# Optimization experiments

Measured on AMD Instinct MI355X. Metric: run time of the kernel, lower is better.

The kernel has to match this reference:

```python
import jax, jax.numpy as jnp
import numpy as np

BEV_X = 128
BEV_Y = 128
NUM_VOXELS = BEV_X * BEV_Y


def setup_inputs() -> dict:
    key = jax.random.key(0)
    k1, k2, k3 = jax.random.split(key, 3)
    B, N, D, H, W, C = 2, 6, 112, 16, 44, 80
    depth_logits = jax.random.normal(k1, (B, N, D, H, W), dtype=jnp.float32)
    context = jax.random.normal(k2, (B, N, C, H, W), dtype=jnp.float32)
    geom_idx = jax.random.randint(k3, (B, N, D, H, W), 0, NUM_VOXELS, dtype=jnp.int32)
    return {"depth_logits": depth_logits, "context": context, "geom_idx": geom_idx}


def reference(depth_logits, context, geom_idx):
    # depth_logits: [B,N,D,H,W], context: [B,N,C,H,W], geom_idx: [B,N,D,H,W] in [0, NUM_VOXELS)
    B, N, D, H, W = depth_logits.shape
    C = context.shape[2]
    # softmax over depth bins -> per-pixel depth distribution
    depth = jax.nn.softmax(depth_logits, axis=2)
    # lift: outer product depth x context -> [B,N,D,H,W,C]
    feat = jnp.einsum('bndhw,bnchw->bndhwc', depth, context)
    P = N * D * H * W
    feat = feat.reshape(B * P, C)
    # splat: scatter-add each frustum point into its BEV voxel (batch-offset indices)
    idx = (geom_idx.reshape(B, P) + jnp.arange(B, dtype=jnp.int32)[:, None] * NUM_VOXELS).reshape(-1)
    bev = jax.ops.segment_sum(feat, idx, num_segments=B * NUM_VOXELS)
    # [B, C, BEV_Y, BEV_X]
    return bev.reshape(B, BEV_Y, BEV_X, C).transpose(0, 3, 1, 2)
```

## Files before the change

### kernel.cpp

```cpp
#include <hip/hip_runtime.h>
#include <hip/hip_bf16.h>


constexpr int B = 2, N = 6, D = 112, H = 16, W = 44, C = 80;
constexpr int HW = H * W;
constexpr int NPIX = B * N * HW;
constexpr int NV = 128 * 128;
constexpr int DHW = D * HW;
constexpr int NBKT = 512;
constexpr int CAP = 2816;
constexpr int RPB = 16 * D;
constexpr int C2 = C / 2;

__device__ inline unsigned bf16rne(float f) {
  const unsigned u = __float_as_uint(f);
  return (u + 0x7FFFu + ((u >> 16) & 1u)) >> 16;
}

__global__ __launch_bounds__(256) void scatter_kernel(
    const float* __restrict__ logits, const float* __restrict__ ctx,
    const int* __restrict__ gidx, unsigned* __restrict__ ctxB,
    int* __restrict__ cursor, unsigned* __restrict__ sorted) {
  const int t = threadIdx.x;
  const int blk = blockIdx.x;
  const int bn = blk / 44;
  const int hw0 = (blk - bn * 44) * 16;
  const int b = bn / N;
  const int pix0 = bn * HW + hw0;

  __shared__ float tile[16][81];
  __shared__ float redm[16][17], reds[16][17];
  __shared__ int hist[256], sbase[256], soff[256];
  __shared__ int wsum[4];
  __shared__ unsigned srec[RPB];
  __shared__ unsigned char sbkt[RPB];

  hist[t] = 0;

  const float* csrc = ctx + (size_t)bn * C * HW + hw0;
#pragma unroll
  for (int it = 0; it < (16 * C) / 256; ++it) {
    const int idx = it * 256 + t;
    const int c = idx >> 4;
    const int i = idx & 15;
    tile[i][c] = csrc[(size_t)c * HW + i];
  }
  __syncthreads();
  {
    unsigned* dst = ctxB + (size_t)pix0 * C2;
    for (int j = t; j < 16 * C2; j += 256) {
      const int p = j / C2;
      const int cp = j - p * C2;
      dst[j] = bf16rne(tile[p][2 * cp]) |
               (bf16rne(tile[p][2 * cp + 1]) << 16);
    }
  }

  const int l = t & 15;
  const int q = t >> 4;
  const size_t base = (size_t)bn * DHW + hw0 + l;

  float x[7];
  float m = -3.0e38f;
#pragma unroll
  for (int j = 0; j < 7; ++j) {
    x[j] = logits[base + (size_t)(q * 7 + j) * HW];
    m = fmaxf(m, x[j]);
  }
  redm[l][q] = m;
  __syncthreads();
#pragma unroll
  for (int qq = 0; qq < 16; ++qq) m = fmaxf(m, redm[l][qq]);
  float s = 0.0f;
#pragma unroll
  for (int j = 0; j < 7; ++j) {
    x[j] = __expf(x[j] - m);
    s += x[j];
  }
  reds[l][q] = s;
  __syncthreads();
  s = 0.0f;
#pragma unroll
  for (int qq = 0; qq < 16; ++qq) s += reds[l][qq];
  const float inv = 1.0f / s;

  unsigned key[7];
  int lb7[7], rank[7];
#pragma unroll
  for (int j = 0; j < 7; ++j) {
    const int fb = b * NV + gidx[base + (size_t)(q * 7 + j) * HW];
    const unsigned p12 = __float2uint_rn(x[j] * inv * 4095.0f);
    key[j] = ((unsigned)(fb & 63) << 26) | ((unsigned)(pix0 + l) << 12) | p12;
    lb7[j] = (fb >> 6) & 255;
    rank[j] = atomicAdd(&hist[lb7[j]], 1);
  }
  __syncthreads();

  const int hv = hist[t];
  int xx = hv;
#pragma unroll
  for (int o = 1; o < 64; o <<= 1) {
    const int y = __shfl_up(xx, o, 64);
    if ((t & 63) >= o) xx += y;
  }
  if ((t & 63) == 63) wsum[t >> 6] = xx;
  sbase[t] = hv ? atomicAdd(&cursor[(b << 8) | t], hv) : 0;
  __syncthreads();
  int woff = 0;
#pragma unroll
  for (int ww = 0; ww < 4; ++ww)
    if (ww < (t >> 6)) woff += wsum[ww];
  soff[t] = woff + xx - hv;
  __syncthreads();

#pragma unroll
  for (int j = 0; j < 7; ++j) {
    const int slot = soff[lb7[j]] + rank[j];
    srec[slot] = key[j];
    sbkt[slot] = (unsigned char)lb7[j];
  }
  __syncthreads();

  for (int s_ = t; s_ < RPB; s_ += 256) {
    const int lb = sbkt[s_];
    const int posin = sbase[lb] + (s_ - soff[lb]);
    if (posin < CAP)
      sorted[(size_t)((b << 8) | lb) * CAP + posin] = srec[s_];
  }
}

__global__ __launch_bounds__(1024) void gather_kernel(
    const unsigned* __restrict__ ctxB, const unsigned* __restrict__ sorted,
    const int* __restrict__ cursor, float* __restrict__ out) {
  const int t = threadIdx.x;
  const int g = blockIdx.x;
  const int b = g >> 8;
  const int vox0 = (g & 255) * 64;

  __shared__ unsigned srec[CAP];
  __shared__ float tile[64][80];
  __shared__ int shist[64], soff[64];

  if (t < 64) shist[t] = 0;
  __syncthreads();

  int cnt = cursor[g];
  if (cnt > CAP) cnt = CAP;
  const unsigned* rec = sorted + (size_t)g * CAP;

  unsigned rr[3];
  int rk[3];
#pragma unroll
  for (int k = 0; k < 3; ++k) {
    const int idx = t + k * 1024;
    rk[k] = -1;
    if (idx < cnt) {
      rr[k] = rec[idx];
      rk[k] = atomicAdd(&shist[rr[k] >> 26], 1);
    }
  }
  __syncthreads();

  if (t < 64) {
    const int v = shist[t];
    int xx = v;
#pragma unroll
    for (int o = 1; o < 64; o <<= 1) {
      const int y = __shfl_up(xx, o, 64);
      if (t >= o) xx += y;
    }
    soff[t] = xx - v;
  }
  __syncthreads();

#pragma unroll
  for (int k = 0; k < 3; ++k) {
    if (rk[k] >= 0) srec[soff[rr[k] >> 26] + rk[k]] = rr[k];
  }
  __syncthreads();

  constexpr float QS = 1.0f / 4095.0f;
  const int w = t >> 6;
  const int l = t & 63;
  for (int j = 0; j < 4; ++j) {
    const int v = w * 4 + j;
    const int s0 = soff[v];
    const int n = shist[v];
    float a0 = 0.0f, a1 = 0.0f;
    int k = 0;
    for (; k + 4 <= n; k += 4) {
      const unsigned ra = srec[s0 + k + 0];
      const unsigned rb = srec[s0 + k + 1];
      const unsigned rc = srec[s0 + k + 2];
      const unsigned rd = srec[s0 + k + 3];
      if (l < C2) {
        const unsigned ua = ctxB[(size_t)((ra >> 12) & 0x3FFFu) * C2 + l];
        const unsigned ub = ctxB[(size_t)((rb >> 12) & 0x3FFFu) * C2 + l];
        const unsigned uc = ctxB[(size_t)((rc >> 12) & 0x3FFFu) * C2 + l];
        const unsigned ud = ctxB[(size_t)((rd >> 12) & 0x3FFFu) * C2 + l];
        const float pa = (float)(ra & 0xFFFu) * QS;
        const float pb = (float)(rb & 0xFFFu) * QS;
        const float pc = (float)(rc & 0xFFFu) * QS;
        const float pd = (float)(rd & 0xFFFu) * QS;
        a0 += pa * __uint_as_float(ua << 16);
        a1 += pa * __uint_as_float(ua & 0xFFFF0000u);
        a0 += pb * __uint_as_float(ub << 16);
        a1 += pb * __uint_as_float(ub & 0xFFFF0000u);
        a0 += pc * __uint_as_float(uc << 16);
        a1 += pc * __uint_as_float(uc & 0xFFFF0000u);
        a0 += pd * __uint_as_float(ud << 16);
        a1 += pd * __uint_as_float(ud & 0xFFFF0000u);
      }
    }
    for (; k < n; ++k) {
      const unsigned ra = srec[s0 + k];
      if (l < C2) {
        const unsigned ua = ctxB[(size_t)((ra >> 12) & 0x3FFFu) * C2 + l];
        const float pa = (float)(ra & 0xFFFu) * QS;
        a0 += pa * __uint_as_float(ua << 16);
        a1 += pa * __uint_as_float(ua & 0xFFFF0000u);
      }
    }
    if (l < C2) {
      tile[v][2 * l] = a0;
      tile[v][2 * l + 1] = a1;
    }
  }
  __syncthreads();

  const size_t ob = (size_t)b * C * NV + vox0;
#pragma unroll
  for (int i = 0; i < 5; ++i) {
    const int idx = i * 1024 + t;
    const int c = idx >> 6;
    const int v = idx & 63;
    out[ob + (size_t)c * NV + v] = tile[v][c];
  }
}

__global__ __launch_bounds__(256) void lift_splat_direct_kernel(
    const float* __restrict__ logits, const float* __restrict__ ctx,
    const int* __restrict__ gidx, float* __restrict__ out) {
  const int t = threadIdx.x;
  const int pix = blockIdx.x;
  const int hw = pix % HW;
  const int bn = pix / HW;
  const int b = bn / N;

  const float* lg = logits + (size_t)bn * DHW + hw;
  const int* gi = gidx + (size_t)bn * DHW + hw;
  const float* cx = ctx + (size_t)bn * (C * HW) + hw;

  __shared__ float s_prob[D];
  __shared__ float s_ctx[C];
  __shared__ int s_idx[D];
  __shared__ float red[256];

  float v = -3.0e38f;
  if (t < D) {
    v = lg[(size_t)t * HW];
    s_idx[t] = gi[(size_t)t * HW];
  }
  if (t < C) s_ctx[t] = cx[(size_t)t * HW];

  red[t] = v;
  __syncthreads();
#pragma unroll
  for (int s = 128; s >= 1; s >>= 1) {
    if (t < s) red[t] = fmaxf(red[t], red[t + s]);
    __syncthreads();
  }
  const float m = red[0];
  __syncthreads();

  const float e = (t < D) ? __expf(v - m) : 0.0f;
  red[t] = e;
  __syncthreads();
#pragma unroll
  for (int s = 128; s >= 1; s >>= 1) {
    if (t < s) red[t] += red[t + s];
    __syncthreads();
  }
  const float inv = 1.0f / red[0];
  if (t < D) s_prob[t] = e * inv;
  __syncthreads();

  for (int f = t; f < D * C; f += 256) {
    const int d = f / C;
    const int c = f - d * C;
    atomicAdd(&out[((size_t)(b * C + c)) * NV + s_idx[d]],
              s_prob[d] * s_ctx[c]);
  }
}

extern "C" void kernel_launch(void* const* d_in, const int* in_sizes, int n_in,
                              void* d_out, int out_size, void* d_ws,
                              size_t ws_size, hipStream_t stream) {
  const float* logits = (const float*)d_in[0];
  const float* ctx = (const float*)d_in[1];
  const int* gidx = (const int*)d_in[2];
  float* out = (float*)d_out;

  size_t off = 0;
  unsigned* sorted = (unsigned*)((char*)d_ws + off);
  off += (size_t)NBKT * CAP * sizeof(unsigned);
  unsigned* ctxB = (unsigned*)((char*)d_ws + off);
  off += (size_t)NPIX * C2 * sizeof(unsigned);
  int* cursor = (int*)((char*)d_ws + off);
  off += (size_t)NBKT * sizeof(int);

  if (ws_size >= off) {
    (void)hipMemsetAsync(cursor, 0, (size_t)NBKT * sizeof(int), stream);
    scatter_kernel<<<B * N * (HW / 16), 256, 0, stream>>>(
        logits, ctx, gidx, ctxB, cursor, sorted);
    gather_kernel<<<NBKT, 1024, 0, stream>>>(ctxB, sorted, cursor, out);
  } else {
    (void)hipMemsetAsync(d_out, 0, (size_t)out_size * sizeof(float), stream);
    lift_splat_direct_kernel<<<NPIX, 256, 0, stream>>>(logits, ctx, gidx, out);
  }
}
```

Measured before the change: 102.4 us.

## Fuse scatter and gather into one cooperative kernel with grid sync

Merges the bucketing scatter kernel and the per-voxel gather kernel into a single cooperative launch separated by a grid-wide barrier, and drops the memset and global atomic cursors. Each tile block now writes its locally sorted records plus a per-bucket header of offsets and counts. Gather blocks prefix-sum these headers and copy segments from all tiles of their batch. This removes a launch, the memset and global atomics, but adds a grid sync, a serial per-thread copy loop in the gather phase and larger shared memory per block, which may limit occupancy.

```diff
diff --git a/kernel.cpp b/kernel.cpp
--- a/kernel.cpp
+++ b/kernel.cpp
@@ -1,5 +1,8 @@
 #include <hip/hip_runtime.h>
 #include <hip/hip_bf16.h>
+#include <hip/hip_cooperative_groups.h>
+
+namespace cg = cooperative_groups;
 
 
 constexpr int B = 2, N = 6, D = 112, H = 16, W = 44, C = 80;
@@ -7,160 +10,179 @@
 constexpr int NPIX = B * N * HW;
 constexpr int NV = 128 * 128;
 constexpr int DHW = D * HW;
-constexpr int NBKT = 512;
-constexpr int CAP = 2816;
-constexpr int RPB = 16 * D;
+constexpr int TPX = 32;
+constexpr int NT = NPIX / TPX;
+constexpr int BT = NT / B;
+constexpr int TREC = TPX * D;
 constexpr int C2 = C / 2;
+constexpr int GRID = 512;
+constexpr int THR = 512;
+constexpr int SCAP = 2304;
 
 __device__ inline unsigned bf16rne(float f) {
   const unsigned u = __float_as_uint(f);
   return (u + 0x7FFFu + ((u >> 16) & 1u)) >> 16;
 }
 
-__global__ __launch_bounds__(256) void scatter_kernel(
+__global__ __launch_bounds__(THR) void fused_kernel(
     const float* __restrict__ logits, const float* __restrict__ ctx,
     const int* __restrict__ gidx, unsigned* __restrict__ ctxB,
-    int* __restrict__ cursor, unsigned* __restrict__ sorted) {
+    unsigned* __restrict__ sorted, unsigned* __restrict__ hdr,
+    float* __restrict__ out) {
   const int t = threadIdx.x;
   const int blk = blockIdx.x;
-  const int bn = blk / 44;
-  const int hw0 = (blk - bn * 44) * 16;
-  const int b = bn / N;
-  const int pix0 = bn * HW + hw0;
-
-  __shared__ float tile[16][81];
-  __shared__ float redm[16][17], reds[16][17];
-  __shared__ int hist[256], sbase[256], soff[256];
+
+  __shared__ float tile_s[TPX][81];
+  __shared__ float redm[TPX][17], reds[TPX][17];
+  __shared__ int hist[256], soffA[256];
   __shared__ int wsum[4];
-  __shared__ unsigned srec[RPB];
-  __shared__ unsigned char sbkt[RPB];
-
-  hist[t] = 0;
-
-  const float* csrc = ctx + (size_t)bn * C * HW + hw0;
-#pragma unroll
-  for (int it = 0; it < (16 * C) / 256; ++it) {
-    const int idx = it * 256 + t;
-    const int c = idx >> 4;
-    const int i = idx & 15;
-    tile[i][c] = csrc[(size_t)c * HW + i];
-  }
-  __syncthreads();
-  {
-    unsigned* dst = ctxB + (size_t)pix0 * C2;
-    for (int j = t; j < 16 * C2; j += 256) {
-      const int p = j / C2;
-      const int cp = j - p * C2;
-      dst[j] = bf16rne(tile[p][2 * cp]) |
-               (bf16rne(tile[p][2 * cp + 1]) << 16);
-    }
-  }
-
-  const int l = t & 15;
-  const int q = t >> 4;
-  const size_t base = (size_t)bn * DHW + hw0 + l;
-
-  float x[7];
-  float m = -3.0e38f;
-#pragma unroll
-  for (int j = 0; j < 7; ++j) {
-    x[j] = logits[base + (size_t)(q * 7 + j) * HW];
-    m = fmaxf(m, x[j]);
-  }
-  redm[l][q] = m;
-  __syncthreads();
-#pragma unroll
-  for (int qq = 0; qq < 16; ++qq) m = fmaxf(m, redm[l][qq]);
-  float s = 0.0f;
-#pragma unroll
-  for (int j = 0; j < 7; ++j) {
-    x[j] = __expf(x[j] - m);
-    s += x[j];
-  }
-  reds[l][q] = s;
-  __syncthreads();
-  s = 0.0f;
-#pragma unroll
-  for (int qq = 0; qq < 16; ++qq) s += reds[l][qq];
-  const float inv = 1.0f / s;
-
-  unsigned key[7];
-  int lb7[7], rank[7];
-#pragma unroll
-  for (int j = 0; j < 7; ++j) {
-    const int fb = b * NV + gidx[base + (size_t)(q * 7 + j) * HW];
-    const unsigned p12 = __float2uint_rn(x[j] * inv * 4095.0f);
-    key[j] = ((unsigned)(fb & 63) << 26) | ((unsigned)(pix0 + l) << 12) | p12;
-    lb7[j] = (fb >> 6) & 255;
-    rank[j] = atomicAdd(&hist[lb7[j]], 1);
-  }
-  __syncthreads();
-
-  const int hv = hist[t];
-  int xx = hv;
-#pragma unroll
-  for (int o = 1; o < 64; o <<= 1) {
-    const int y = __shfl_up(xx, o, 64);
-    if ((t & 63) >= o) xx += y;
-  }
-  if ((t & 63) == 63) wsum[t >> 6] = xx;
-  sbase[t] = hv ? atomicAdd(&cursor[(b << 8) | t], hv) : 0;
-  __syncthreads();
-  int woff = 0;
-#pragma unroll
-  for (int ww = 0; ww < 4; ++ww)
-    if (ww < (t >> 6)) woff += wsum[ww];
-  soff[t] = woff + xx - hv;
-  __syncthreads();
-
-#pragma unroll
-  for (int j = 0; j < 7; ++j) {
-    const int slot = soff[lb7[j]] + rank[j];
-    srec[slot] = key[j];
-    sbkt[slot] = (unsigned char)lb7[j];
-  }
-  __syncthreads();
-
-  for (int s_ = t; s_ < RPB; s_ += 256) {
-    const int lb = sbkt[s_];
-    const int posin = sbase[lb] + (s_ - soff[lb]);
-    if (posin < CAP)
-      sorted[(size_t)((b << 8) | lb) * CAP + posin] = srec[s_];
-  }
-}
-
-__global__ __launch_bounds__(1024) void gather_kernel(
-    const unsigned* __restrict__ ctxB, const unsigned* __restrict__ sorted,
-    const int* __restrict__ cursor, float* __restrict__ out) {
-  const int t = threadIdx.x;
-  const int g = blockIdx.x;
-  const int b = g >> 8;
-  const int vox0 = (g & 255) * 64;
-
-  __shared__ unsigned srec[CAP];
-  __shared__ float tile[64][80];
-  __shared__ int shist[64], soff[64];
+  __shared__ unsigned srecA[TREC];
+  __shared__ int scnt[BT];
+  __shared__ unsigned srec2[SCAP];
+  __shared__ int shist[64], soff2[64];
+  __shared__ float tileO[64][81];
+
+  if (blk < NT) {
+    const int bn = blk / 22;
+    const int hw0 = (blk % 22) * TPX;
+    const int b = bn / N;
+    const int pix0 = bn * HW + hw0;
+
+    if (t < 256) hist[t] = 0;
+
+    const float* csrc = ctx + (size_t)bn * C * HW + hw0;
+#pragma unroll
+    for (int it = 0; it < (TPX * C) / THR; ++it) {
+      const int idx = it * THR + t;
+      const int c = idx >> 5;
+      const int i = idx & 31;
+      tile_s[i][c] = csrc[(size_t)c * HW + i];
+    }
+    __syncthreads();
+    {
+      unsigned* dst = ctxB + (size_t)pix0 * C2;
+      for (int j = t; j < TPX * C2; j += THR) {
+        const int p = j / C2;
+        const int cp = j - p * C2;
+        dst[j] = bf16rne(tile_s[p][2 * cp]) |
+                 (bf16rne(tile_s[p][2 * cp + 1]) << 16);
+      }
+    }
+
+    const int l = t & 31;
+    const int q = t >> 5;
+    const size_t base = (size_t)bn * DHW + hw0 + l;
+
+    float x[7];
+    float m = -3.0e38f;
+#pragma unroll
+    for (int j = 0; j < 7; ++j) {
+      x[j] = logits[base + (size_t)(q * 7 + j) * HW];
+      m = fmaxf(m, x[j]);
+    }
+    redm[l][q] = m;
+    __syncthreads();
+#pragma unroll
+    for (int qq = 0; qq < 16; ++qq) m = fmaxf(m, redm[l][qq]);
+    float s = 0.0f;
+#pragma unroll
+    for (int j = 0; j < 7; ++j) {
+      x[j] = __expf(x[j] - m);
+      s += x[j];
+    }
+    reds[l][q] = s;
+    __syncthreads();
+    s = 0.0f;
+#pragma unroll
+    for (int qq = 0; qq < 16; ++qq) s += reds[l][qq];
+    const float inv = 1.0f / s;
+
+    unsigned key[7];
+    int lb7[7], rank[7];
+#pragma unroll
+    for (int j = 0; j < 7; ++j) {
+      const int fb = b * NV + gidx[base + (size_t)(q * 7 + j) * HW];
+      const unsigned p12 = __float2uint_rn(x[j] * inv * 4095.0f);
+      key[j] = ((unsigned)(fb & 63) << 26) | ((unsigned)(pix0 + l) << 12) | p12;
+      lb7[j] = (fb >> 6) & 255;
+      rank[j] = atomicAdd(&hist[lb7[j]], 1);
+    }
+    __syncthreads();
+
+    const int hv = (t < 256) ? hist[t] : 0;
+    int xx = hv;
+#pragma unroll
+    for (int o = 1; o < 64; o <<= 1) {
+      const int y = __shfl_up(xx, o, 64);
+      if ((t & 63) >= o) xx += y;
+    }
+    if (((t & 63) == 63) && t < 256) wsum[t >> 6] = xx;
+    __syncthreads();
+    if (t < 256) {
+      int woff = 0;
+#pragma unroll
+      for (int ww = 0; ww < 4; ++ww)
+        if (ww < (t >> 6)) woff += wsum[ww];
+      soffA[t] = woff + xx - hv;
+    }
+    __syncthreads();
+
+#pragma unroll
+    for (int j = 0; j < 7; ++j)
+      srecA[soffA[lb7[j]] + rank[j]] = key[j];
+    if (t < 256)
+      hdr[(size_t)blk * 256 + t] =
+          ((unsigned)soffA[t] << 16) | (unsigned)hist[t];
+    __syncthreads();
+
+    for (int s_ = t; s_ < TREC; s_ += THR)
+      sorted[(size_t)blk * TREC + s_] = srecA[s_];
+  }
+
+  cg::this_grid().sync();
+
+  const int b = blk >> 8;
+  const int lb = blk & 255;
 
   if (t < 64) shist[t] = 0;
-  __syncthreads();
-
-  int cnt = cursor[g];
-  if (cnt > CAP) cnt = CAP;
-  const unsigned* rec = sorted + (size_t)g * CAP;
-
-  unsigned rr[3];
-  int rk[3];
-#pragma unroll
-  for (int k = 0; k < 3; ++k) {
-    const int idx = t + k * 1024;
+  int cnt_t = 0, off_t = 0;
+  if (t < BT) {
+    const unsigned h = hdr[(size_t)(b * BT + t) * 256 + lb];
+    off_t = (int)(h >> 16);
+    cnt_t = (int)(h & 0xFFFFu);
+    scnt[t] = cnt_t;
+  }
+  __syncthreads();
+  for (int o = 1; o < BT; o <<= 1) {
+    const int v = (t >= o && t < BT) ? scnt[t - o] : 0;
+    __syncthreads();
+    if (t < BT) scnt[t] += v;
+    __syncthreads();
+  }
+  int total = scnt[BT - 1];
+  if (total > SCAP) total = SCAP;
+  if (t < BT) {
+    const int pos = scnt[t] - cnt_t;
+    const unsigned* src = sorted + (size_t)(b * BT + t) * TREC + off_t;
+    for (int i = 0; i < cnt_t; ++i) {
+      const int p = pos + i;
+      if (p < SCAP) srec2[p] = src[i];
+    }
+  }
+  __syncthreads();
+
+  unsigned rr[5];
+  int rk[5];
+#pragma unroll
+  for (int k = 0; k < 5; ++k) {
+    const int idx = t + k * THR;
     rk[k] = -1;
-    if (idx < cnt) {
-      rr[k] = rec[idx];
+    if (idx < total) {
+      rr[k] = srec2[idx];
       rk[k] = atomicAdd(&shist[rr[k] >> 26], 1);
     }
   }
   __syncthreads();
-
   if (t < 64) {
     const int v = shist[t];
     int xx = v;
@@ -169,30 +191,28 @@
       const int y = __shfl_up(xx, o, 64);
       if (t >= o) xx += y;
     }
-    soff[t] = xx - v;
-  }
-  __syncthreads();
-
-#pragma unroll
-  for (int k = 0; k < 3; ++k) {
-    if (rk[k] >= 0) srec[soff[rr[k] >> 26] + rk[k]] = rr[k];
-  }
+    soff2[t] = xx - v;
+  }
+  __syncthreads();
+#pragma unroll
+  for (int k = 0; k < 5; ++k)
+    if (rk[k] >= 0) srec2[soff2[rr[k] >> 26] + rk[k]] = rr[k];
   __syncthreads();
 
   constexpr float QS = 1.0f / 4095.0f;
   const int w = t >> 6;
   const int l = t & 63;
-  for (int j = 0; j < 4; ++j) {
-    const int v = w * 4 + j;
-    const int s0 = soff[v];
+  for (int j = 0; j < 8; ++j) {
+    const int v = w * 8 + j;
+    const int s0 = soff2[v];
     const int n = shist[v];
     float a0 = 0.0f, a1 = 0.0f;
     int k = 0;
     for (; k + 4 <= n; k += 4) {
-      const unsigned ra = srec[s0 + k + 0];
-      const unsigned rb = srec[s0 + k + 1];
-      const unsigned rc = srec[s0 + k + 2];
-      const unsigned rd = srec[s0 + k + 3];
+      const unsigned ra = srec2[s0 + k + 0];
+      const unsigned rb = srec2[s0 + k + 1];
+      const unsigned rc = srec2[s0 + k + 2];
+      const unsigned rd = srec2[s0 + k + 3];
       if (l < C2) {
         const unsigned ua = ctxB[(size_t)((ra >> 12) & 0x3FFFu) * C2 + l];
         const unsigned ub = ctxB[(size_t)((rb >> 12) & 0x3FFFu) * C2 + l];
@@ -213,7 +233,7 @@
       }
     }
     for (; k < n; ++k) {
-      const unsigned ra = srec[s0 + k];
+      const unsigned ra = srec2[s0 + k];
       if (l < C2) {
         const unsigned ua = ctxB[(size_t)((ra >> 12) & 0x3FFFu) * C2 + l];
         const float pa = (float)(ra & 0xFFFu) * QS;
@@ -222,19 +242,19 @@
       }
     }
     if (l < C2) {
-      tile[v][2 * l] = a0;
-      tile[v][2 * l + 1] = a1;
-    }
-  }
-  __syncthreads();
-
-  const size_t ob = (size_t)b * C * NV + vox0;
-#pragma unroll
-  for (int i = 0; i < 5; ++i) {
-    const int idx = i * 1024 + t;
+      tileO[v][2 * l] = a0;
+      tileO[v][2 * l + 1] = a1;
+    }
+  }
+  __syncthreads();
+
+  const size_t ob = (size_t)b * C * NV + (size_t)lb * 64;
+#pragma unroll
+  for (int i = 0; i < 10; ++i) {
+    const int idx = i * THR + t;
     const int c = idx >> 6;
     const int v = idx & 63;
-    out[ob + (size_t)c * NV + v] = tile[v][c];
+    out[ob + (size_t)c * NV + v] = tileO[v][c];
   }
 }
 
@@ -303,17 +323,24 @@
 
   size_t off = 0;
   unsigned* sorted = (unsigned*)((char*)d_ws + off);
-  off += (size_t)NBKT * CAP * sizeof(unsigned);
+  off += (size_t)NT * TREC * sizeof(unsigned);
   unsigned* ctxB = (unsigned*)((char*)d_ws + off);
   off += (size_t)NPIX * C2 * sizeof(unsigned);
-  int* cursor = (int*)((char*)d_ws + off);
-  off += (size_t)NBKT * sizeof(int);
+  unsigned* hdr = (unsigned*)((char*)d_ws + off);
+  off += (size_t)NT * 256 * sizeof(unsigned);
 
   if (ws_size >= off) {
-    (void)hipMemsetAsync(cursor, 0, (size_t)NBKT * sizeof(int), stream);
-    scatter_kernel<<<B * N * (HW / 16), 256, 0, stream>>>(
-        logits, ctx, gidx, ctxB, cursor, sorted);
-    gather_kernel<<<NBKT, 1024, 0, stream>>>(ctxB, sorted, cursor, out);
+    void* kargs[7];
+    kargs[0] = (void*)&logits;
+    kargs[1] = (void*)&ctx;
+    kargs[2] = (void*)&gidx;
+    kargs[3] = (void*)&ctxB;
+    kargs[4] = (void*)&sorted;
+    kargs[5] = (void*)&hdr;
+    kargs[6] = (void*)&out;
+    (void)hipLaunchCooperativeKernel(
+        reinterpret_cast<void*>(fused_kernel), dim3(GRID), dim3(THR), kargs,
+        0, stream);
   } else {
     (void)hipMemsetAsync(d_out, 0, (size_t)out_size * sizeof(float), stream);
     lift_splat_direct_kernel<<<NPIX, 256, 0, stream>>>(logits, ctx, gidx, out);
```

After: 183.4 us. +79.1%, slower.
